# Optimization experiments

Measured on AMD Instinct MI355X. Metric: run time of the kernel, lower is better.

The kernel has to match this reference:

```python
import jax, jax.numpy as jnp
import numpy as np

B, D_MODEL, D_SAE, K = 8192, 768, 16384, 64


def setup_inputs() -> dict:
    key = jax.random.key(0)
    k1, k2, k3 = jax.random.split(key, 3)
    return {
        "x": jax.random.normal(k1, (B, D_MODEL), dtype=jnp.float32),
        "W_enc": jax.random.normal(k2, (D_MODEL, D_SAE), dtype=jnp.float32) * 0.02,
        "b_enc": jnp.zeros((D_SAE,), dtype=jnp.float32),
        "W_dec": jax.random.normal(k3, (D_SAE, D_MODEL), dtype=jnp.float32) * 0.02,
        "b_dec": jnp.zeros((D_MODEL,), dtype=jnp.float32),
        "k": K,
    }


def reference(x, W_enc, b_enc, W_dec, b_dec, k):
    # encode: [B, d_sae]
    pre_relu = jax.nn.relu(x @ W_enc + b_enc)
    if k >= pre_relu.shape[-1]:
        z = pre_relu
    else:
        topk_vals, topk_idx = jax.lax.top_k(pre_relu, k)  # [B, k]
        z = jnp.zeros_like(pre_relu)
        z = jnp.take_along_axis(
            jnp.zeros_like(pre_relu), topk_idx, axis=-1
        )  # placeholder not needed; use scatter via at[]
        rows = jnp.arange(pre_relu.shape[0])[:, None]  # [B, 1]
        z = jnp.zeros_like(pre_relu).at[rows, topk_idx].set(topk_vals)
    recon = z @ W_dec + b_dec
    return (z, recon)
```

## Files before the change

kernel.cpp:

```cpp
#include <hip/hip_runtime.h>
#include <cstdint>

#define NROWS 8192
#define DM    768
#define DS    16384
#define PREB_STRIDE 32768

typedef __attribute__((ext_vector_type(8))) short          bf16x8;
typedef __attribute__((ext_vector_type(8))) unsigned short u16x8;
typedef __attribute__((ext_vector_type(4))) float          f32x4;

__device__ __forceinline__ unsigned short f2bf(float f) {
  unsigned u = __float_as_uint(f);
  unsigned r = u + 0x7fffu + ((u >> 16) & 1u);
  return (unsigned short)(r >> 16);
}
__device__ __forceinline__ float bf2f(unsigned short us) {
  return __uint_as_float(((unsigned)us) << 16);
}

#define GLOAD_LDS16(g, l)                                                     \
  __builtin_amdgcn_global_load_lds(                                           \
      (const __attribute__((address_space(1))) void*)(g),                     \
      (__attribute__((address_space(3))) void*)(l), 16, 0, 0)


__global__ __launch_bounds__(256) void cvt_x_bf16(const float* __restrict__ x,
                                                  unsigned short* __restrict__ xb) {
  int i = blockIdx.x * 256 + threadIdx.x;
  float4 v = ((const float4*)x)[i];
  ushort4 o;
  o.x = f2bf(v.x); o.y = f2bf(v.y); o.z = f2bf(v.z); o.w = f2bf(v.w);
  ((ushort4*)xb)[i] = o;
}

__global__ __launch_bounds__(256) void cvt_wd_bf16(const float* __restrict__ wd,
                                                   unsigned short* __restrict__ wdb) {
  int i = blockIdx.x * 256 + threadIdx.x;
  float4 v = ((const float4*)wd)[i];
  ushort4 o;
  o.x = f2bf(v.x); o.y = f2bf(v.y); o.z = f2bf(v.z); o.w = f2bf(v.w);
  ((ushort4*)wdb)[i] = o;
}

__global__ __launch_bounds__(256) void transpose_w(const float* __restrict__ We,
                                                   float* __restrict__ WTf,
                                                   unsigned short* __restrict__ WTb) {
  __shared__ float t[32][33];
  const int c0 = blockIdx.x * 32;
  const int r0 = blockIdx.y * 32;
  const int tx = threadIdx.x & 31, ty = threadIdx.x >> 5;
#pragma unroll
  for (int i = 0; i < 4; ++i)
    t[ty + i * 8][tx] = We[(size_t)(r0 + ty + i * 8) * DS + c0 + tx];
  __syncthreads();
#pragma unroll
  for (int i = 0; i < 4; ++i) {
    float v = t[tx][ty + i * 8];
    size_t o = (size_t)(c0 + ty + i * 8) * DM + r0 + tx;
    WTf[o] = v;
    WTb[o] = f2bf(v);
  }
}

__global__ __launch_bounds__(256) void sae_encode_bf16(
    const unsigned short* __restrict__ xb,
    const unsigned short* __restrict__ WTb,
    const float* __restrict__ be,
    unsigned short* __restrict__ preb,
    float* __restrict__ zfull)
{
  __shared__ __align__(16) short As[128 * 64];
  __shared__ __align__(16) short Bs[128 * 64];

  const int tid  = threadIdx.x;
  const int lane = tid & 63;
  const int w    = tid >> 6;
  const int wm   = w >> 1, wn = w & 1;
  const int m0   = blockIdx.y * 128, n0 = blockIdx.x * 128;
  const int l15  = lane & 15, q = lane >> 4, l7 = lane & 7;

  f32x4 acc[4][4];
  const f32x4 zero4 = {0.f, 0.f, 0.f, 0.f};
#pragma unroll
  for (int i = 0; i < 4; ++i)
#pragma unroll
    for (int j = 0; j < 4; ++j) acc[i][j] = zero4;

  for (int k0 = 0; k0 < DM; k0 += 64) {
#pragma unroll
    for (int j = 0; j < 4; ++j) {
      int pj  = (w << 8) + (j << 6) + lane;
      int m   = pj >> 3, gp = pj & 7;
      int col = ((gp ^ (m & 7)) << 3);
      const unsigned short* ga = xb  + (size_t)(m0 + m) * DM + k0 + col;
      const unsigned short* gb = WTb + (size_t)(n0 + m) * DM + k0 + col;
      int ldsoff = ((w << 8) + (j << 6)) << 4;
      GLOAD_LDS16(ga, (char*)As + ldsoff);
      GLOAD_LDS16(gb, (char*)Bs + ldsoff);
    }
    __syncthreads();

#pragma unroll
    for (int h = 0; h < 2; ++h) {
      const int gsw = (((h * 4 + q) ^ l7) << 4);
      bf16x8 af[4], bfr[4];
#pragma unroll
      for (int t = 0; t < 4; ++t) {
        af[t]  = *(const bf16x8*)((const char*)As + (wm * 64 + t * 16 + l15) * 128 + gsw);
        bfr[t] = *(const bf16x8*)((const char*)Bs + (wn * 64 + t * 16 + l15) * 128 + gsw);
      }
#pragma unroll
      for (int mf = 0; mf < 4; ++mf)
#pragma unroll
        for (int nf = 0; nf < 4; ++nf)
          acc[mf][nf] = __builtin_amdgcn_mfma_f32_16x16x32_bf16(
              af[mf], bfr[nf], acc[mf][nf], 0, 0, 0);
    }
    __syncthreads();
  }

#pragma unroll
  for (int nf = 0; nf < 4; ++nf) {
    const int gcol = n0 + wn * 64 + nf * 16 + l15;
    const float bias = be[gcol];
#pragma unroll
    for (int mf = 0; mf < 4; ++mf) {
#pragma unroll
      for (int r = 0; r < 4; ++r) {
        int grow = m0 + wm * 64 + mf * 16 + q * 4 + r;
        preb[(size_t)grow * PREB_STRIDE + gcol] = f2bf(acc[mf][nf][r] + bias);
      }
    }
  }

  if (n0 >= DS / 2) {
    const float4 z4 = make_float4(0.f, 0.f, 0.f, 0.f);
    const int r0w = tid >> 5;
    const int c0w = (tid & 31) << 2;
#pragma unroll
    for (int i = 0; i < 16; ++i) {
      *(float4*)(zfull + (size_t)(m0 + r0w + i * 8) * DS + n0 + c0w) = z4;
    }
  }
}

#define MARGIN 0.04f
#define FINE_LO 0x3C800000u
#define FINE_HI 0x40800000u
#define HICAP 256
#define BDCAP 512
#define SELCAP 160

__global__ __launch_bounds__(256) void sae_topk_fused(
    float* __restrict__ z,
    float* __restrict__ recon,
    const float* __restrict__ x,
    const float* __restrict__ WTf,
    const float* __restrict__ be,
    const float* __restrict__ Wd,
    const unsigned short* __restrict__ WdB,
    const float* __restrict__ bd,
    const int* __restrict__ kptr)
{
  const int row = blockIdx.x;
  const int tid = threadIdx.x;
  int k = *kptr; if (k < 1) k = 1; if (k > 128) k = 128;

  float* zrow = z + (size_t)row * DS;
  const unsigned short* zrowb = (const unsigned short*)zrow;

  __shared__ int   fine[2048];
  __shared__ int   part[256];
  __shared__ int   s_above, s_pos;
  __shared__ uint2 sh_LU;
  __shared__ float xs[DM];
  __shared__ int   hi_idx[HICAP];
  __shared__ float hi_val[HICAP];
  __shared__ int   bd_idx[BDCAP];
  __shared__ float cex[BDCAP];
  __shared__ int   s_nh, s_nb;
  __shared__ int   sidx[SELCAP];
  __shared__ float sval[SELCAP];

#pragma unroll
  for (int i = 0; i < 8; ++i) fine[tid + i * 256] = 0;
  if (tid == 0) { s_above = 0; s_pos = 0; s_nh = 0; s_nb = 0; }
  for (int i = tid; i < DM; i += 256) xs[i] = x[(size_t)row * DM + i];
  __syncthreads();

  int above_c = 0, pos_c = 0;
  {
    const u16x8* srcb = (const u16x8*)zrowb;
#pragma unroll
    for (int it = 0; it < 8; ++it) {
      int idx = tid + it * 256;
      u16x8 v = srcb[idx];
#pragma unroll
      for (int e = 0; e < 8; ++e) {
        unsigned short us = (unsigned short)v[e];
        if (us > 0 && us < 0x8000) {
          ++pos_c;
          unsigned b = ((unsigned)us) << 16;
          if (b >= FINE_HI) ++above_c;
          else if (b >= FINE_LO) atomicAdd(&fine[(b >> 15) - (FINE_LO >> 15)], 1);
        }
      }
    }
  }
  if (above_c) atomicAdd(&s_above, above_c);
  if (pos_c)   atomicAdd(&s_pos, pos_c);
  __syncthreads();

  int p = 0;
#pragma unroll
  for (int i = 0; i < 8; ++i) p += fine[tid * 8 + i];
  part[tid] = p;
  __syncthreads();
  for (int off = 1; off < 256; off <<= 1) {
    int v = part[tid];
    int add = (tid + off < 256) ? part[tid + off] : 0;
    __syncthreads();
    part[tid] = v + add;
    __syncthreads();
  }
  const int tot_fine = part[0];

  if (s_pos < k) {
    if (tid == 0) sh_LU = make_uint2(0u, 0u);
  } else if (s_above >= k) {
    if (tid == 0) sh_LU = make_uint2(FINE_HI, 0x7F7FFFFFu);
  } else if (s_above + tot_fine < k) {
    if (tid == 0) sh_LU = make_uint2(0u, FINE_LO);
  } else {
    int nxt = (tid == 255) ? 0 : part[tid + 1];
    if (s_above + part[tid] >= k && (tid == 255 || s_above + nxt < k)) {
      int acc = s_above + nxt;
      int bin = 0;
      for (int i = 7; i >= 0; --i) {
        acc += fine[tid * 8 + i];
        if (acc >= k) { bin = tid * 8 + i; break; }
      }
      unsigned L = (unsigned)(bin + (int)(FINE_LO >> 15)) << 15;
      sh_LU = make_uint2(L, L + (1u << 15));
    }
  }
  __syncthreads();

  unsigned ulo, uhi;
  {
    const uint2 t2 = sh_LU;
    if (t2.y == 0u) {
      ulo = 0u; uhi = 0u;
    } else {
      float Lf = __uint_as_float(t2.x) - MARGIN;
      ulo = (Lf > 0.f) ? __float_as_uint(Lf) : 0u;
      float Uf = __uint_as_float(t2.y) + MARGIN;
      uhi = __float_as_uint(Uf);
    }
  }

  {
    const u16x8* srcb = (const u16x8*)zrowb;
#pragma unroll
    for (int it = 0; it < 8; ++it) {
      int idx = tid + it * 256;
      u16x8 v = srcb[idx];
#pragma unroll
      for (int e = 0; e < 8; ++e) {
        unsigned short us = (unsigned short)v[e];
        if (us > 0 && us < 0x8000) {
          unsigned b = ((unsigned)us) << 16;
          if (b > uhi) {
            int pp = atomicAdd(&s_nh, 1);
            if (pp < HICAP) { hi_idx[pp] = idx * 8 + e; hi_val[pp] = __uint_as_float(b); }
          } else if (b > ulo) {
            int pp = atomicAdd(&s_nb, 1);
            if (pp < BDCAP) bd_idx[pp] = idx * 8 + e;
          }
        }
      }
    }
  }
  {
    const float4 z4 = make_float4(0.f, 0.f, 0.f, 0.f);
    float4* p4 = (float4*)zrow;
#pragma unroll
    for (int jj = 0; jj < 8; ++jj) p4[tid + jj * 256] = z4;
  }
  __syncthreads();
  const int nh = (s_nh < HICAP) ? s_nh : HICAP;
  const int nb = (s_nb < BDCAP) ? s_nb : BDCAP;

  for (int c = tid; c < nb; c += 256) {
    const float* wcol = WTf + (size_t)bd_idx[c] * DM;
    float s = 0.f;
#pragma unroll 8
    for (int i = 0; i < DM; ++i) s = fmaf(xs[i], wcol[i], s);
    cex[c] = s + be[bd_idx[c]];
  }
  __syncthreads();

  int nh_kept, need;
  if (nh <= k) {
    nh_kept = nh;
    need = k - nh;
    for (int t = tid; t < nh; t += 256) {
      int myi = hi_idx[t];
      int r = 0;
      for (int c = 0; c < nh; ++c) r += (hi_idx[c] < myi);
      sidx[r] = myi; sval[r] = hi_val[t];
    }
  } else {
    nh_kept = k;
    need = 0;
    for (int t = tid; t < nh; t += 256) {
      float er = hi_val[t];
      int myi = hi_idx[t];
      int r = 0;
      for (int c = 0; c < nh; ++c)
        r += (hi_val[c] > er) || (hi_val[c] == er && hi_idx[c] < myi);
      if (r < k) { sidx[r] = myi; sval[r] = er; }
    }
  }
  __syncthreads();

  for (int t = tid; t < nb; t += 256) {
    float er = fmaxf(cex[t], 0.f);
    int myi = bd_idx[t];
    int r = 0;
    for (int c = 0; c < nb; ++c) {
      float ec = fmaxf(cex[c], 0.f);
      r += (ec > er) || (ec == er && bd_idx[c] < myi);
    }
    if (r < need) { sidx[nh_kept + r] = myi; sval[nh_kept + r] = er; }
  }
  __syncthreads();

  const int nsel = nh_kept + (need < nb ? need : nb);

  if (tid < nsel) zrow[sidx[tid]] = sval[tid];

  float a0 = bd[tid], a1 = bd[tid + 256], a2 = bd[tid + 512];
  if (WdB) {
    for (int r = 0; r < nsel; ++r) {
      float v = sval[r];
      const unsigned short* wr = WdB + (size_t)sidx[r] * DM;
      a0 = fmaf(v, bf2f(wr[tid]),       a0);
      a1 = fmaf(v, bf2f(wr[tid + 256]), a1);
      a2 = fmaf(v, bf2f(wr[tid + 512]), a2);
    }
  } else {
    for (int r = 0; r < nsel; ++r) {
      float v = sval[r];
      const float* wr = Wd + (size_t)sidx[r] * DM;
      a0 = fmaf(v, wr[tid],       a0);
      a1 = fmaf(v, wr[tid + 256], a1);
      a2 = fmaf(v, wr[tid + 512], a2);
    }
  }
  float* rr = recon + (size_t)row * DM;
  rr[tid] = a0; rr[tid + 256] = a1; rr[tid + 512] = a2;
}

#define BM 128
#define BN 128
#define BK 32

__global__ __launch_bounds__(256) void sae_encode_gemm(
    const float* __restrict__ x, const float* __restrict__ We,
    const float* __restrict__ be, float* __restrict__ pre)
{
  __shared__ float As2[BK][BM];
  __shared__ float Bs2[BK][BN];

  const int tid = threadIdx.x;
  const int bx  = blockIdx.x;
  const int by  = blockIdx.y;
  const int c0  = (tid & 15) * 4;
  const int r0  = (tid >> 4) * 4;

  float acc[2][2][4][4];
#pragma unroll
  for (int p = 0; p < 2; ++p)
#pragma unroll
    for (int qq = 0; qq < 2; ++qq)
#pragma unroll
      for (int i = 0; i < 4; ++i)
#pragma unroll
        for (int j = 0; j < 4; ++j) acc[p][qq][i][j] = 0.f;

  const float* xblk = x  + (size_t)by * BM * DM;
  const float* wblk = We + (size_t)bx * BN;

  for (int k0 = 0; k0 < DM; k0 += BK) {
#pragma unroll
    for (int i = 0; i < 4; ++i) {
      int s  = tid + i * 256;
      int m  = s >> 3;
      int kk4 = (s & 7) << 2;
      float4 v = *(const float4*)(xblk + (size_t)m * DM + (k0 + kk4));
      int cs = m ^ kk4;
      As2[kk4 + 0][cs] = v.x;
      As2[kk4 + 1][cs] = v.y;
      As2[kk4 + 2][cs] = v.z;
      As2[kk4 + 3][cs] = v.w;
    }
#pragma unroll
    for (int i = 0; i < 4; ++i) {
      int s  = tid + i * 256;
      int kk = s >> 5;
      int n  = (s & 31) << 2;
      *(float4*)&Bs2[kk][n] = *(const float4*)(wblk + (size_t)(k0 + kk) * DS + n);
    }
    __syncthreads();
#pragma unroll 4
    for (int kk = 0; kk < BK; ++kk) {
      const int kkm = kk & 0x1C;
      const int ra  = r0 ^ kkm;
      float4 a0 = *(const float4*)&As2[kk][ra];
      float4 a1 = *(const float4*)&As2[kk][ra + 64];
      float4 b0 = *(const float4*)&Bs2[kk][c0];
      float4 b1 = *(const float4*)&Bs2[kk][c0 + 64];
      float av[2][4] = {{a0.x, a0.y, a0.z, a0.w}, {a1.x, a1.y, a1.z, a1.w}};
      float bv[2][4] = {{b0.x, b0.y, b0.z, b0.w}, {b1.x, b1.y, b1.z, b1.w}};
#pragma unroll
      for (int p = 0; p < 2; ++p)
#pragma unroll
        for (int qq = 0; qq < 2; ++qq)
#pragma unroll
          for (int i = 0; i < 4; ++i)
#pragma unroll
            for (int j = 0; j < 4; ++j)
              acc[p][qq][i][j] = fmaf(av[p][i], bv[qq][j], acc[p][qq][i][j]);
    }
    __syncthreads();
  }

  const int row0 = by * BM + r0;
  const int col0 = bx * BN + c0;
  float bias[2][4];
#pragma unroll
  for (int qq = 0; qq < 2; ++qq)
#pragma unroll
    for (int j = 0; j < 4; ++j) bias[qq][j] = be[col0 + qq * 64 + j];
#pragma unroll
  for (int p = 0; p < 2; ++p)
#pragma unroll
    for (int i = 0; i < 4; ++i) {
      float* dst = pre + (size_t)(row0 + p * 64 + i) * DS + col0;
#pragma unroll
      for (int qq = 0; qq < 2; ++qq) {
        float4 o;
        o.x = fmaxf(acc[p][qq][i][0] + bias[qq][0], 0.f);
        o.y = fmaxf(acc[p][qq][i][1] + bias[qq][1], 0.f);
        o.z = fmaxf(acc[p][qq][i][2] + bias[qq][2], 0.f);
        o.w = fmaxf(acc[p][qq][i][3] + bias[qq][3], 0.f);
        *(float4*)(dst + qq * 64) = o;
      }
    }
}

__global__ __launch_bounds__(256) void sae_topk_decode(
    float* __restrict__ z, float* __restrict__ recon,
    const float* __restrict__ Wd, const float* __restrict__ bd,
    const int* __restrict__ kptr)
{
  const int row = blockIdx.x;
  const int tid = threadIdx.x;
  int k = *kptr;
  if (k < 1) k = 1;
  if (k > 1024) k = 1024;

  float* zrow = z + (size_t)row * DS;

  unsigned u[64];
  {
    const float4* src = (const float4*)zrow;
#pragma unroll
    for (int jj = 0; jj < 16; ++jj) {
      float4 v = src[tid + jj * 256];
      u[jj * 4 + 0] = (v.x > 0.f) ? __float_as_uint(v.x) : 0u;
      u[jj * 4 + 1] = (v.y > 0.f) ? __float_as_uint(v.y) : 0u;
      u[jj * 4 + 2] = (v.z > 0.f) ? __float_as_uint(v.z) : 0u;
      u[jj * 4 + 3] = (v.w > 0.f) ? __float_as_uint(v.w) : 0u;
    }
  }

  __shared__ int red[8];
  unsigned tbits = 0;
  for (int bit = 30; bit >= 0; --bit) {
    unsigned cand = tbits | (1u << bit);
    int c = 0;
#pragma unroll
    for (int j = 0; j < 64; ++j) c += (u[j] >= cand);
#pragma unroll
    for (int off = 32; off > 0; off >>= 1) c += __shfl_down(c, off, 64);
    if ((tid & 63) == 0) red[tid >> 6] = c;
    __syncthreads();
    int tot = red[0] + red[1] + red[2] + red[3];
    __syncthreads();
    if (tot >= k) tbits = cand;
  }

  int cnt_gt = 0, cnt_eq = 0;
  if (tbits != 0) {
    int c1 = 0, c2 = 0;
#pragma unroll
    for (int j = 0; j < 64; ++j) { c1 += (u[j] > tbits); c2 += (u[j] == tbits); }
#pragma unroll
    for (int off = 32; off > 0; off >>= 1) {
      c1 += __shfl_down(c1, off, 64);
      c2 += __shfl_down(c2, off, 64);
    }
    if ((tid & 63) == 0) { red[tid >> 6] = c1; red[4 + (tid >> 6)] = c2; }
    __syncthreads();
    cnt_gt = red[0] + red[1] + red[2] + red[3];
    cnt_eq = red[4] + red[5] + red[6] + red[7];
    __syncthreads();
  }
  const int needed = k - cnt_gt;

  __shared__ int eq_n;
  __shared__ int eq_keep;
  __shared__ int eq_idx[256];
  const bool rare = (tbits != 0) && (cnt_eq > needed);
  if (rare) {
    if (tid == 0) eq_n = 0;
    __syncthreads();
#pragma unroll
    for (int jj = 0; jj < 16; ++jj)
#pragma unroll
      for (int c = 0; c < 4; ++c) {
        int j = jj * 4 + c;
        if (u[j] == tbits) {
          int p = atomicAdd(&eq_n, 1);
          if (p < 256) eq_idx[p] = (tid + jj * 256) * 4 + c;
        }
      }
    __syncthreads();
    if (tid == 0) {
      int n = eq_n < 256 ? eq_n : 256;
      for (int a = 1; a < n; ++a) {
        int key = eq_idx[a]; int b = a - 1;
        while (b >= 0 && eq_idx[b] > key) { eq_idx[b + 1] = eq_idx[b]; --b; }
        eq_idx[b + 1] = key;
      }
      int kp = needed < n ? needed : n;
      eq_keep = kp < 0 ? 0 : kp;
    }
    __syncthreads();
  }

  unsigned long long mask = 0ull;
#pragma unroll
  for (int jj = 0; jj < 16; ++jj)
#pragma unroll
    for (int c = 0; c < 4; ++c) {
      int j = jj * 4 + c;
      bool s;
      if (tbits == 0) {
        s = (u[j] > 0u);
      } else if (u[j] > tbits) {
        s = true;
      } else if (u[j] == tbits) {
        if (!rare) s = true;
        else {
          int idx = (tid + jj * 256) * 4 + c;
          s = false;
          for (int e = 0; e < eq_keep; ++e)
            if (eq_idx[e] == idx) { s = true; break; }
        }
      } else s = false;
      if (s) mask |= (1ull << j);
    }
  const int mycount = __popcll(mask);

  __shared__ int scan[256];
  scan[tid] = mycount;
  __syncthreads();
  for (int off = 1; off < 256; off <<= 1) {
    int v = scan[tid];
    int add = (tid >= off) ? scan[tid - off] : 0;
    __syncthreads();
    scan[tid] = v + add;
    __syncthreads();
  }
  const int total = scan[255];
  int pos = scan[tid] - mycount;

  __shared__ float s_val[1024];
  __shared__ int   s_idx[1024];
  {
    float4* dst = (float4*)zrow;
#pragma unroll
    for (int jj = 0; jj < 16; ++jj) {
      float4 wv;
      float* wp = (float*)&wv;
#pragma unroll
      for (int c = 0; c < 4; ++c) {
        int j = jj * 4 + c;
        bool s = (mask >> j) & 1ull;
        float val = __uint_as_float(u[j]);
        wp[c] = s ? val : 0.f;
        if (s && pos < 1024) {
          s_idx[pos] = (tid + jj * 256) * 4 + c;
          s_val[pos] = val;
          ++pos;
        }
      }
      dst[tid + jj * 256] = wv;
    }
  }
  __syncthreads();

  float a0 = bd[tid], a1 = bd[tid + 256], a2 = bd[tid + 512];
  const int n = total < 1024 ? total : 1024;
#pragma unroll 4
  for (int i = 0; i < n; ++i) {
    float v = s_val[i];
    const float* wr = Wd + (size_t)s_idx[i] * DM;
    a0 = fmaf(v, wr[tid],       a0);
    a1 = fmaf(v, wr[tid + 256], a1);
    a2 = fmaf(v, wr[tid + 512], a2);
  }
  float* rr = recon + (size_t)row * DM;
  rr[tid] = a0; rr[tid + 256] = a1; rr[tid + 512] = a2;
}

extern "C" void kernel_launch(void* const* d_in, const int* in_sizes, int n_in,
                              void* d_out, int out_size, void* d_ws, size_t ws_size,
                              hipStream_t stream) {
  (void)in_sizes; (void)n_in; (void)out_size;

  const float* x     = (const float*)d_in[0];
  const float* W_enc = (const float*)d_in[1];
  const float* b_enc = (const float*)d_in[2];
  const float* W_dec = (const float*)d_in[3];
  const float* b_dec = (const float*)d_in[4];
  const int*   kp    = (const int*)d_in[5];

  float* z     = (float*)d_out;
  float* recon = z + (size_t)NROWS * DS;

  const size_t sz_WTf = (size_t)DS * DM * 4;
  const size_t sz_WTb = (size_t)DS * DM * 2;
  const size_t sz_xb  = (size_t)NROWS * DM * 2;
  const size_t sz_WdB = (size_t)DS * DM * 2;
  const size_t need_small = sz_WTf + sz_WTb + sz_xb;
  const size_t need_big   = need_small + sz_WdB;

  if (ws_size >= need_small) {
    float*          WTf = (float*)d_ws;
    unsigned short* WTb = (unsigned short*)((char*)d_ws + sz_WTf);
    unsigned short* xb  = (unsigned short*)((char*)d_ws + sz_WTf + sz_WTb);
    unsigned short* WdB = nullptr;

    cvt_x_bf16<<<(NROWS * DM) / (4 * 256), 256, 0, stream>>>(x, xb);
    if (ws_size >= need_big) {
      WdB = (unsigned short*)((char*)d_ws + need_small);
      cvt_wd_bf16<<<((size_t)DS * DM) / (4 * 256), 256, 0, stream>>>(W_dec, WdB);
    }
    transpose_w<<<dim3(DS / 32, DM / 32), 256, 0, stream>>>(W_enc, WTf, WTb);
    sae_encode_bf16<<<dim3(DS / 128, NROWS / 128), 256, 0, stream>>>(
        xb, WTb, b_enc, (unsigned short*)z, z);
    sae_topk_fused<<<NROWS, 256, 0, stream>>>(z, recon, x, WTf, b_enc,
                                              W_dec, WdB, b_dec, kp);
  } else {
    sae_encode_gemm<<<dim3(DS / BN, NROWS / BM), 256, 0, stream>>>(x, W_enc, b_enc, z);
    sae_topk_decode<<<NROWS, 256, 0, stream>>>(z, recon, W_dec, b_dec, kp);
  }
}
```

Baseline: 857.7 us.

## Split fused top-k kernel into select and finish kernels via workspace lists

Splits the per-row top-k plus decode kernel into two launches. The first builds the histogram threshold, writes high and borderline candidate lists to the workspace and zeroes the z row. The second reloads those lists, recomputes borderline values in fp32, ranks them, scatters into z and runs the decode. The goal is lower shared memory and register use per kernel to raise occupancy, at the cost of an extra launch and global round-trips for the candidate lists.

```diff
diff --git a/kernel.cpp b/kernel.cpp
--- a/kernel.cpp
+++ b/kernel.cpp
@@ -23,6 +23,13 @@
   __builtin_amdgcn_global_load_lds(                                           \
       (const __attribute__((address_space(1))) void*)(g),                     \
       (__attribute__((address_space(3))) void*)(l), 16, 0, 0)
+
+#define MARGIN 0.04f
+#define FINE_LO 0x3C800000u
+#define FINE_HI 0x40800000u
+#define HICAP 256
+#define BDCAP 512
+#define SELCAP 160
 
 
 __global__ __launch_bounds__(256) void cvt_x_bf16(const float* __restrict__ x,
@@ -145,22 +152,13 @@
   }
 }
 
-#define MARGIN 0.04f
-#define FINE_LO 0x3C800000u
-#define FINE_HI 0x40800000u
-#define HICAP 256
-#define BDCAP 512
-#define SELCAP 160
-
-__global__ __launch_bounds__(256) void sae_topk_fused(
+
+__global__ __launch_bounds__(256) void sae_select2(
     float* __restrict__ z,
-    float* __restrict__ recon,
-    const float* __restrict__ x,
-    const float* __restrict__ WTf,
-    const float* __restrict__ be,
-    const float* __restrict__ Wd,
-    const unsigned short* __restrict__ WdB,
-    const float* __restrict__ bd,
+    int*   __restrict__ hiIdxAll,
+    float* __restrict__ hiValAll,
+    int*   __restrict__ bdIdxAll,
+    uint2* __restrict__ cnts,
     const int* __restrict__ kptr)
 {
   const int row = blockIdx.x;
@@ -172,21 +170,12 @@
 
   __shared__ int   fine[2048];
   __shared__ int   part[256];
-  __shared__ int   s_above, s_pos;
+  __shared__ int   s_above, s_pos, s_nh, s_nb;
   __shared__ uint2 sh_LU;
-  __shared__ float xs[DM];
-  __shared__ int   hi_idx[HICAP];
-  __shared__ float hi_val[HICAP];
-  __shared__ int   bd_idx[BDCAP];
-  __shared__ float cex[BDCAP];
-  __shared__ int   s_nh, s_nb;
-  __shared__ int   sidx[SELCAP];
-  __shared__ float sval[SELCAP];
 
 #pragma unroll
   for (int i = 0; i < 8; ++i) fine[tid + i * 256] = 0;
   if (tid == 0) { s_above = 0; s_pos = 0; s_nh = 0; s_nb = 0; }
-  for (int i = tid; i < DM; i += 256) xs[i] = x[(size_t)row * DM + i];
   __syncthreads();
 
   int above_c = 0, pos_c = 0;
@@ -250,9 +239,250 @@
   unsigned ulo, uhi;
   {
     const uint2 t2 = sh_LU;
-    if (t2.y == 0u) {
-      ulo = 0u; uhi = 0u;
-    } else {
+    if (t2.y == 0u) { ulo = 0u; uhi = 0u; }
+    else {
+      float Lf = __uint_as_float(t2.x) - MARGIN;
+      ulo = (Lf > 0.f) ? __float_as_uint(Lf) : 0u;
+      float Uf = __uint_as_float(t2.y) + MARGIN;
+      uhi = __float_as_uint(Uf);
+    }
+  }
+
+  int*   hiI = hiIdxAll + (size_t)row * HICAP;
+  float* hiV = hiValAll + (size_t)row * HICAP;
+  int*   bdI = bdIdxAll + (size_t)row * BDCAP;
+
+  {
+    const u16x8* srcb = (const u16x8*)zrowb;
+#pragma unroll
+    for (int it = 0; it < 8; ++it) {
+      int idx = tid + it * 256;
+      u16x8 v = srcb[idx];
+#pragma unroll
+      for (int e = 0; e < 8; ++e) {
+        unsigned short us = (unsigned short)v[e];
+        if (us > 0 && us < 0x8000) {
+          unsigned b = ((unsigned)us) << 16;
+          if (b > uhi) {
+            int pp = atomicAdd(&s_nh, 1);
+            if (pp < HICAP) { hiI[pp] = idx * 8 + e; hiV[pp] = __uint_as_float(b); }
+          } else if (b > ulo) {
+            int pp = atomicAdd(&s_nb, 1);
+            if (pp < BDCAP) bdI[pp] = idx * 8 + e;
+          }
+        }
+      }
+    }
+  }
+  {
+    const float4 z4 = make_float4(0.f, 0.f, 0.f, 0.f);
+    float4* p4 = (float4*)zrow;
+#pragma unroll
+    for (int jj = 0; jj < 8; ++jj) p4[tid + jj * 256] = z4;
+  }
+  __syncthreads();
+  if (tid == 0) cnts[row] = make_uint2((unsigned)s_nh, (unsigned)s_nb);
+}
+
+__global__ __launch_bounds__(256) void sae_finish(
+    float* __restrict__ z,
+    float* __restrict__ recon,
+    const float* __restrict__ x,
+    const float* __restrict__ WTf,
+    const float* __restrict__ be,
+    const unsigned short* __restrict__ WdB,
+    const float* __restrict__ bd,
+    const int*   __restrict__ hiIdxAll,
+    const float* __restrict__ hiValAll,
+    const int*   __restrict__ bdIdxAll,
+    const uint2* __restrict__ cnts,
+    const int* __restrict__ kptr)
+{
+  const int row = blockIdx.x;
+  const int tid = threadIdx.x;
+  int k = *kptr; if (k < 1) k = 1; if (k > 128) k = 128;
+
+  float* zrow = z + (size_t)row * DS;
+
+  __shared__ float xs[DM];
+  __shared__ int   hi_idx[HICAP];
+  __shared__ float hi_val[HICAP];
+  __shared__ int   bd_idx[BDCAP];
+  __shared__ float cex[BDCAP];
+  __shared__ int   sidx[SELCAP];
+  __shared__ float sval[SELCAP];
+
+  const uint2 c2 = cnts[row];
+  const int nh = ((int)c2.x < HICAP) ? (int)c2.x : HICAP;
+  const int nb = ((int)c2.y < BDCAP) ? (int)c2.y : BDCAP;
+
+  for (int i = tid; i < DM; i += 256) xs[i] = x[(size_t)row * DM + i];
+  {
+    const int*   hiI = hiIdxAll + (size_t)row * HICAP;
+    const float* hiV = hiValAll + (size_t)row * HICAP;
+    const int*   bdI = bdIdxAll + (size_t)row * BDCAP;
+    for (int i = tid; i < nh; i += 256) { hi_idx[i] = hiI[i]; hi_val[i] = hiV[i]; }
+    for (int i = tid; i < nb; i += 256) { bd_idx[i] = bdI[i]; }
+  }
+  __syncthreads();
+
+  for (int c = tid; c < nb; c += 256) {
+    const float* wcol = WTf + (size_t)bd_idx[c] * DM;
+    float s = 0.f;
+#pragma unroll 8
+    for (int i = 0; i < DM; ++i) s = fmaf(xs[i], wcol[i], s);
+    cex[c] = s + be[bd_idx[c]];
+  }
+  __syncthreads();
+
+  int nh_kept, need;
+  if (nh <= k) {
+    nh_kept = nh;
+    need = k - nh;
+    for (int t = tid; t < nh; t += 256) {
+      int myi = hi_idx[t];
+      int r = 0;
+      for (int c = 0; c < nh; ++c) r += (hi_idx[c] < myi);
+      sidx[r] = myi; sval[r] = hi_val[t];
+    }
+  } else {
+    nh_kept = k;
+    need = 0;
+    for (int t = tid; t < nh; t += 256) {
+      float er = hi_val[t];
+      int myi = hi_idx[t];
+      int r = 0;
+      for (int c = 0; c < nh; ++c)
+        r += (hi_val[c] > er) || (hi_val[c] == er && hi_idx[c] < myi);
+      if (r < k) { sidx[r] = myi; sval[r] = er; }
+    }
+  }
+  __syncthreads();
+
+  for (int t = tid; t < nb; t += 256) {
+    float er = fmaxf(cex[t], 0.f);
+    int myi = bd_idx[t];
+    int r = 0;
+    for (int c = 0; c < nb; ++c) {
+      float ec = fmaxf(cex[c], 0.f);
+      r += (ec > er) || (ec == er && bd_idx[c] < myi);
+    }
+    if (r < need) { sidx[nh_kept + r] = myi; sval[nh_kept + r] = er; }
+  }
+  __syncthreads();
+
+  const int nsel = nh_kept + (need < nb ? need : nb);
+
+  if (tid < nsel) zrow[sidx[tid]] = sval[tid];
+
+  float a0 = bd[tid], a1 = bd[tid + 256], a2 = bd[tid + 512];
+  for (int r = 0; r < nsel; ++r) {
+    float v = sval[r];
+    const unsigned short* wr = WdB + (size_t)sidx[r] * DM;
+    a0 = fmaf(v, bf2f(wr[tid]),       a0);
+    a1 = fmaf(v, bf2f(wr[tid + 256]), a1);
+    a2 = fmaf(v, bf2f(wr[tid + 512]), a2);
+  }
+  float* rr = recon + (size_t)row * DM;
+  rr[tid] = a0; rr[tid + 256] = a1; rr[tid + 512] = a2;
+}
+
+__global__ __launch_bounds__(256) void sae_topk_fused(
+    float* __restrict__ z, float* __restrict__ recon,
+    const float* __restrict__ x, const float* __restrict__ WTf,
+    const float* __restrict__ be, const float* __restrict__ Wd,
+    const unsigned short* __restrict__ WdB, const float* __restrict__ bd,
+    const int* __restrict__ kptr)
+{
+  const int row = blockIdx.x;
+  const int tid = threadIdx.x;
+  int k = *kptr; if (k < 1) k = 1; if (k > 128) k = 128;
+
+  float* zrow = z + (size_t)row * DS;
+  const unsigned short* zrowb = (const unsigned short*)zrow;
+
+  __shared__ int   fine[2048];
+  __shared__ int   part[256];
+  __shared__ int   s_above, s_pos;
+  __shared__ uint2 sh_LU;
+  __shared__ float xs[DM];
+  __shared__ int   hi_idx[HICAP];
+  __shared__ float hi_val[HICAP];
+  __shared__ int   bd_idx[BDCAP];
+  __shared__ float cex[BDCAP];
+  __shared__ int   s_nh, s_nb;
+  __shared__ int   sidx[SELCAP];
+  __shared__ float sval[SELCAP];
+
+#pragma unroll
+  for (int i = 0; i < 8; ++i) fine[tid + i * 256] = 0;
+  if (tid == 0) { s_above = 0; s_pos = 0; s_nh = 0; s_nb = 0; }
+  for (int i = tid; i < DM; i += 256) xs[i] = x[(size_t)row * DM + i];
+  __syncthreads();
+
+  int above_c = 0, pos_c = 0;
+  {
+    const u16x8* srcb = (const u16x8*)zrowb;
+#pragma unroll
+    for (int it = 0; it < 8; ++it) {
+      int idx = tid + it * 256;
+      u16x8 v = srcb[idx];
+#pragma unroll
+      for (int e = 0; e < 8; ++e) {
+        unsigned short us = (unsigned short)v[e];
+        if (us > 0 && us < 0x8000) {
+          ++pos_c;
+          unsigned b = ((unsigned)us) << 16;
+          if (b >= FINE_HI) ++above_c;
+          else if (b >= FINE_LO) atomicAdd(&fine[(b >> 15) - (FINE_LO >> 15)], 1);
+        }
+      }
+    }
+  }
+  if (above_c) atomicAdd(&s_above, above_c);
+  if (pos_c)   atomicAdd(&s_pos, pos_c);
+  __syncthreads();
+
+  int p = 0;
+#pragma unroll
+  for (int i = 0; i < 8; ++i) p += fine[tid * 8 + i];
+  part[tid] = p;
+  __syncthreads();
+  for (int off = 1; off < 256; off <<= 1) {
+    int v = part[tid];
+    int add = (tid + off < 256) ? part[tid + off] : 0;
+    __syncthreads();
+    part[tid] = v + add;
+    __syncthreads();
+  }
+  const int tot_fine = part[0];
+
+  if (s_pos < k) {
+    if (tid == 0) sh_LU = make_uint2(0u, 0u);
+  } else if (s_above >= k) {
+    if (tid == 0) sh_LU = make_uint2(FINE_HI, 0x7F7FFFFFu);
+  } else if (s_above + tot_fine < k) {
+    if (tid == 0) sh_LU = make_uint2(0u, FINE_LO);
+  } else {
+    int nxt = (tid == 255) ? 0 : part[tid + 1];
+    if (s_above + part[tid] >= k && (tid == 255 || s_above + nxt < k)) {
+      int acc = s_above + nxt;
+      int bin = 0;
+      for (int i = 7; i >= 0; --i) {
+        acc += fine[tid * 8 + i];
+        if (acc >= k) { bin = tid * 8 + i; break; }
+      }
+      unsigned L = (unsigned)(bin + (int)(FINE_LO >> 15)) << 15;
+      sh_LU = make_uint2(L, L + (1u << 15));
+    }
+  }
+  __syncthreads();
+
+  unsigned ulo, uhi;
+  {
+    const uint2 t2 = sh_LU;
+    if (t2.y == 0u) { ulo = 0u; uhi = 0u; }
+    else {
       float Lf = __uint_as_float(t2.x) - MARGIN;
       ulo = (Lf > 0.f) ? __float_as_uint(Lf) : 0u;
       float Uf = __uint_as_float(t2.y) + MARGIN;
@@ -338,7 +568,6 @@
   __syncthreads();
 
   const int nsel = nh_kept + (need < nb ? need : nb);
-
   if (tid < nsel) zrow[sidx[tid]] = sval[tid];
 
   float a0 = bd[tid], a1 = bd[tid + 256], a2 = bd[tid + 512];
@@ -643,12 +872,17 @@
   float* z     = (float*)d_out;
   float* recon = z + (size_t)NROWS * DS;
 
-  const size_t sz_WTf = (size_t)DS * DM * 4;
-  const size_t sz_WTb = (size_t)DS * DM * 2;
-  const size_t sz_xb  = (size_t)NROWS * DM * 2;
-  const size_t sz_WdB = (size_t)DS * DM * 2;
+  const size_t sz_WTf  = (size_t)DS * DM * 4;
+  const size_t sz_WTb  = (size_t)DS * DM * 2;
+  const size_t sz_xb   = (size_t)NROWS * DM * 2;
+  const size_t sz_WdB  = (size_t)DS * DM * 2;
+  const size_t sz_hiI  = (size_t)NROWS * HICAP * 4;
+  const size_t sz_hiV  = (size_t)NROWS * HICAP * 4;
+  const size_t sz_bdI  = (size_t)NROWS * BDCAP * 4;
+  const size_t sz_cnt  = (size_t)NROWS * 8;
   const size_t need_small = sz_WTf + sz_WTb + sz_xb;
   const size_t need_big   = need_small + sz_WdB;
+  const size_t need_lists = need_big + sz_hiI + sz_hiV + sz_bdI + sz_cnt;
 
   if (ws_size >= need_small) {
     float*          WTf = (float*)d_ws;
@@ -664,8 +898,19 @@
     transpose_w<<<dim3(DS / 32, DM / 32), 256, 0, stream>>>(W_enc, WTf, WTb);
     sae_encode_bf16<<<dim3(DS / 128, NROWS / 128), 256, 0, stream>>>(
         xb, WTb, b_enc, (unsigned short*)z, z);
-    sae_topk_fused<<<NROWS, 256, 0, stream>>>(z, recon, x, WTf, b_enc,
-                                              W_dec, WdB, b_dec, kp);
+
+    if (ws_size >= need_lists) {
+      int*   hiI = (int*)((char*)d_ws + need_big);
+      float* hiV = (float*)((char*)d_ws + need_big + sz_hiI);
+      int*   bdI = (int*)((char*)d_ws + need_big + sz_hiI + sz_hiV);
+      uint2* cnt = (uint2*)((char*)d_ws + need_big + sz_hiI + sz_hiV + sz_bdI);
+      sae_select2<<<NROWS, 256, 0, stream>>>(z, hiI, hiV, bdI, cnt, kp);
+      sae_finish<<<NROWS, 256, 0, stream>>>(z, recon, x, WTf, b_enc, WdB, b_dec,
+                                            hiI, hiV, bdI, cnt, kp);
+    } else {
+      sae_topk_fused<<<NROWS, 256, 0, stream>>>(z, recon, x, WTf, b_enc,
+                                                W_dec, WdB, b_dec, kp);
+    }
   } else {
     sae_encode_gemm<<<dim3(DS / BN, NROWS / BM), 256, 0, stream>>>(x, W_enc, b_enc, z);
     sae_topk_decode<<<NROWS, 256, 0, stream>>>(z, recon, W_dec, b_dec, kp);
```

After: 869.5 us. Within noise of the previous version (+1.4%).
